# Kernel optimization log

Measured on AMD Instinct MI355X. Metric: run time of the kernel, lower is better.

The kernel has to match this reference:

```python
import jax, jax.numpy as jnp
import numpy as np

B, S, H = 2, 2048, 768
NH, HD = 12, 64
I = 1152
EPS = 1e-5
ROPE_BASE = 10000.0
MAX_POS = 8192


def _layernorm(x, w, b):
    mu = jnp.mean(x, axis=-1, keepdims=True)
    var = jnp.mean(jnp.square(x - mu), axis=-1, keepdims=True)
    return (x - mu) / jnp.sqrt(var + EPS) * w + b


def _rope_tables():
    pos = jnp.arange(MAX_POS, dtype=jnp.float32)
    theta = 1.0 / (ROPE_BASE ** (jnp.arange(0, HD, 2, dtype=jnp.float32) / HD))
    ang = pos[:, None] * theta  # [MAX_POS, HD//2]
    return jnp.cos(ang), jnp.sin(ang)


def _apply_rope(x, cos, sin):
    # x: [B, NH, S, HD]; cos/sin: [B, 1, S, HD//2]; interleaved pair rotation
    x2 = x.reshape(*x.shape[:-1], HD // 2, 2)
    x0, x1 = x2[..., 0], x2[..., 1]
    rot = jnp.stack([x0 * cos - x1 * sin, x1 * cos + x0 * sin], axis=-1)
    return rot.reshape(x.shape)


def setup_inputs() -> dict:
    key = jax.random.key(0)
    ks = jax.random.split(key, 8)
    std = 0.02
    return {
        "hidden_states": jax.random.normal(ks[0], (B, S, H), dtype=jnp.float32),
        "attention_mask": jnp.zeros((B, 1, S, S), dtype=jnp.float32),
        "sliding_window_mask": jnp.zeros((B, 1, S, S), dtype=jnp.float32),
        "position_ids": jnp.tile(jnp.arange(S, dtype=jnp.int32)[None, :], (B, 1)),
        "qkv_w": jax.random.normal(ks[1], (3 * H, H), dtype=jnp.float32) * std,
        "o_w": jax.random.normal(ks[2], (H, H), dtype=jnp.float32) * std,
        "attn_norm_w": jnp.ones((H,), dtype=jnp.float32),
        "attn_norm_b": jnp.zeros((H,), dtype=jnp.float32),
        "mlp_norm_w": jnp.ones((H,), dtype=jnp.float32),
        "mlp_norm_b": jnp.zeros((H,), dtype=jnp.float32),
        "wi_w": jax.random.normal(ks[3], (2 * I, H), dtype=jnp.float32) * std,
        "wi_b": jnp.zeros((2 * I,), dtype=jnp.float32),
        "wo_w": jax.random.normal(ks[4], (H, I), dtype=jnp.float32) * std,
        "wo_b": jnp.zeros((H,), dtype=jnp.float32),
    }


def reference(hidden_states, attention_mask, sliding_window_mask, position_ids,
              qkv_w, o_w, attn_norm_w, attn_norm_b, mlp_norm_w, mlp_norm_b,
              wi_w, wi_b, wo_w, wo_b):
    # --- attention block (layer_id != 0 -> pre-LN) ---
    x = _layernorm(hidden_states, attn_norm_w, attn_norm_b)
    qkv = jnp.einsum('bsh,oh->bso', x, qkv_w)          # [B,S,3H] (no bias)
    qkv = qkv.reshape(B, S, 3, NH, HD)
    qkv = jnp.transpose(qkv, (0, 3, 2, 1, 4))          # [B,NH,3,S,HD]
    q, k, v = qkv[:, :, 0], qkv[:, :, 1], qkv[:, :, 2]

    cos_t, sin_t = _rope_tables()
    cos = cos_t[position_ids][:, None]                 # [B,1,S,HD//2]
    sin = sin_t[position_ids][:, None]
    q = _apply_rope(q, cos, sin)
    k = _apply_rope(k, cos, sin)

    scale = HD ** -0.5
    scores = jnp.einsum('bhqd,bhkd->bhqk', q, k) * scale
    scores = scores + attention_mask + sliding_window_mask
    probs = jax.nn.softmax(scores, axis=-1)
    ctx = jnp.einsum('bhqk,bhkd->bhqd', probs, v)      # [B,NH,S,HD]
    ctx = jnp.transpose(ctx, (0, 2, 1, 3)).reshape(B, S, H)
    attn_out = jnp.einsum('bsh,oh->bso', ctx, o_w)
    hidden = hidden_states + attn_out

    # --- GeGLU MLP block ---
    y = _layernorm(hidden, mlp_norm_w, mlp_norm_b)
    h = jax.nn.gelu(jnp.einsum('bsh,oh->bso', y, wi_w) + wi_b, approximate=False)
    gated = h[..., 0::2] * h[..., 1::2]                # strided gelu-gate split
    mlp_out = jnp.einsum('bsi,oi->bso', gated, wo_w) + wo_b
    return hidden + mlp_out
```

## Files before the change

kernel.cpp:

```cpp
#include <hip/hip_runtime.h>
#include <hip/hip_bf16.h>
#include <math.h>

#define B_  2
#define S_  2048
#define H_  768
#define NH_ 12
#define HD_ 64
#define I_  1152
#define LOG2E 1.4426950408889634f
#define SCALE_L2E 0.18033688011112042f

typedef __bf16 bf16;
typedef __bf16 bf16x8 __attribute__((ext_vector_type(8)));
typedef float  f32x4  __attribute__((ext_vector_type(4)));
typedef float  f32x16 __attribute__((ext_vector_type(16)));
typedef float  f32x2  __attribute__((ext_vector_type(2)));
typedef unsigned u32x2 __attribute__((ext_vector_type(2)));
typedef unsigned u32x4 __attribute__((ext_vector_type(4)));

__device__ __forceinline__ void gll16(const void* g, void* l) {
  __builtin_amdgcn_global_load_lds((const __attribute__((address_space(1))) void*)g,
                                   (__attribute__((address_space(3))) void*)l, 16, 0, 0);
}

__device__ __forceinline__ unsigned pack_bf16(float a, float b) {
  union { bf16 e[2]; unsigned u; } r;
  r.e[0] = (bf16)a; r.e[1] = (bf16)b;
  return r.u;
}

__device__ __forceinline__ void plswap(unsigned &a, unsigned &b) {
  asm volatile("v_permlane32_swap_b32 %0, %1" : "+v"(a), "+v"(b));
}
__device__ __forceinline__ float halfmax(float x) {
  unsigned a = __builtin_bit_cast(unsigned, x), b = a;
  plswap(a, b);
  return fmaxf(__builtin_bit_cast(float, a), __builtin_bit_cast(float, b));
}
__device__ __forceinline__ float halfsum(float x) {
  unsigned a = __builtin_bit_cast(unsigned, x), b = a;
  plswap(a, b);
  return __builtin_bit_cast(float, a) + __builtin_bit_cast(float, b);
}

__global__ void cvt_f32_bf16(const float* __restrict__ in, bf16* __restrict__ out, int n4) {
  int i = blockIdx.x * 256 + threadIdx.x;
  if (i >= n4) return;
  float4 v = ((const float4*)in)[i];
  union { bf16 e[4]; uint2 u; } r;
  r.e[0] = (bf16)v.x; r.e[1] = (bf16)v.y; r.e[2] = (bf16)v.z; r.e[3] = (bf16)v.w;
  ((uint2*)out)[i] = r.u;
}

__global__ __launch_bounds__(256) void combine_mask2(const float* __restrict__ a,
                                                     const float* __restrict__ b,
                                                     bf16* __restrict__ E,
                                                     unsigned* __restrict__ flags) {
  const int kt = blockIdx.x, qi = blockIdx.y, bb = blockIdx.z, tid = threadIdx.x;
  float sm[8][4];
  bool ok = true;
#pragma unroll
  for (int c = 0; c < 8; ++c) {
    int idx4 = c * 256 + tid;
    int r = idx4 >> 4, col = (idx4 & 15) * 4;
    size_t g = ((size_t)(bb * S_) + qi * 128 + r) * S_ + kt * 64 + col;
    float4 x = *(const float4*)(a + g);
    float4 y = *(const float4*)(b + g);
    sm[c][0] = x.x + y.x; sm[c][1] = x.y + y.y;
    sm[c][2] = x.z + y.z; sm[c][3] = x.w + y.w;
    ok = ok && (sm[c][0] == 0.f) && (sm[c][1] == 0.f) && (sm[c][2] == 0.f) && (sm[c][3] == 0.f);
  }
  __shared__ unsigned sh[4];
  unsigned long long bal = __ballot(ok);
  if ((tid & 63) == 0) sh[tid >> 6] = (bal == ~0ull) ? 1u : 0u;
  __syncthreads();
  unsigned flag = sh[0] & sh[1] & sh[2] & sh[3];
  if (tid == 0) flags[(bb * 16 + qi) * 32 + kt] = flag;
  if (!flag) {
#pragma unroll
    for (int c = 0; c < 8; ++c) {
      int idx4 = c * 256 + tid;
      int r = idx4 >> 4, col = (idx4 & 15) * 4;
      size_t g = ((size_t)(bb * S_) + qi * 128 + r) * S_ + kt * 64 + col;
      union { bf16 e[4]; uint2 u; } w;
      w.e[0] = (bf16)__expf(sm[c][0]); w.e[1] = (bf16)__expf(sm[c][1]);
      w.e[2] = (bf16)__expf(sm[c][2]); w.e[3] = (bf16)__expf(sm[c][3]);
      *(uint2*)(E + g) = w.u;
    }
  }
}

__global__ __launch_bounds__(256) void ln_bf16(const float* __restrict__ in,
                                               const float* __restrict__ w,
                                               const float* __restrict__ bia,
                                               bf16* __restrict__ out) {
  int row = blockIdx.x, tid = threadIdx.x;
  const float* x = in + (size_t)row * H_;
  float v0 = x[tid], v1 = x[tid + 256], v2 = x[tid + 512];
  float s = v0 + v1 + v2;
  float q = v0 * v0 + v1 * v1 + v2 * v2;
  for (int o = 1; o < 64; o <<= 1) { s += __shfl_xor(s, o); q += __shfl_xor(q, o); }
  __shared__ float rs[4], rq[4];
  if ((tid & 63) == 0) { rs[tid >> 6] = s; rq[tid >> 6] = q; }
  __syncthreads();
  s = rs[0] + rs[1] + rs[2] + rs[3];
  q = rq[0] + rq[1] + rq[2] + rq[3];
  float mu = s * (1.f / H_);
  float var = q * (1.f / H_) - mu * mu;
  float rstd = rsqrtf(var + 1e-5f);
  bf16* orow = out + (size_t)row * H_;
  orow[tid]       = (bf16)((v0 - mu) * rstd * w[tid]       + bia[tid]);
  orow[tid + 256] = (bf16)((v1 - mu) * rstd * w[tid + 256] + bia[tid + 256]);
  orow[tid + 512] = (bf16)((v2 - mu) * rstd * w[tid + 512] + bia[tid + 512]);
}

template<bool BIAS, bool RES>
__global__ __launch_bounds__(256) void gemm128(const bf16* __restrict__ A,
                                               const bf16* __restrict__ W,
                                               float* __restrict__ C,
                                               const float* __restrict__ bias,
                                               const float* __restrict__ res,
                                               int M, int N, int K) {
  __shared__ bf16 As[128 * 32];
  __shared__ bf16 Bs[128 * 32];
  const int tid = threadIdx.x, lane = tid & 63, wv = tid >> 6;
  const int bm = blockIdx.y * 128, bn = blockIdx.x * 128;
  const int wr = (wv >> 1) * 64, wc = (wv & 1) * 64;
  const int l15 = lane & 15, lg = lane >> 4;

  f32x4 acc[4][4] = {};

  const int srow = tid >> 2, scc = (tid & 3) * 8;
  const bf16* aSrc0 = A + (size_t)(bm + srow) * K + scc;
  const bf16* aSrc1 = A + (size_t)(bm + 64 + srow) * K + scc;
  const bf16* bSrc0 = W + (size_t)(bn + srow) * K + scc;
  const bf16* bSrc1 = W + (size_t)(bn + 64 + srow) * K + scc;
  bf16* aDst0 = As + (size_t)tid * 8;
  bf16* aDst1 = As + (size_t)(256 + tid) * 8;
  bf16* bDst0 = Bs + (size_t)tid * 8;
  bf16* bDst1 = Bs + (size_t)(256 + tid) * 8;

  for (int k0 = 0; k0 < K; k0 += 32) {
    __syncthreads();
    gll16(aSrc0 + k0, aDst0);
    gll16(aSrc1 + k0, aDst1);
    gll16(bSrc0 + k0, bDst0);
    gll16(bSrc1 + k0, bDst1);
    __syncthreads();
    bf16x8 af[4], bfr[4];
#pragma unroll
    for (int i = 0; i < 4; ++i)
      af[i] = *(const bf16x8*)&As[(wr + i * 16 + l15) * 32 + lg * 8];
#pragma unroll
    for (int j = 0; j < 4; ++j)
      bfr[j] = *(const bf16x8*)&Bs[(wc + j * 16 + l15) * 32 + lg * 8];
#pragma unroll
    for (int i = 0; i < 4; ++i)
#pragma unroll
      for (int j = 0; j < 4; ++j)
        acc[i][j] = __builtin_amdgcn_mfma_f32_16x16x32_bf16(af[i], bfr[j], acc[i][j], 0, 0, 0);
  }

  const int r0 = lg * 4;
#pragma unroll
  for (int i = 0; i < 4; ++i) {
#pragma unroll
    for (int j = 0; j < 4; ++j) {
      int col = bn + wc + j * 16 + l15;
      float bv = BIAS ? bias[col] : 0.f;
#pragma unroll
      for (int r = 0; r < 4; ++r) {
        int row = bm + wr + i * 16 + r0 + r;
        float v = acc[i][j][r] + bv;
        if (RES) v += res[(size_t)row * N + col];
        C[(size_t)row * N + col] = v;
      }
    }
  }
}

__global__ void rope_split(const float* __restrict__ qkv, const int* __restrict__ pid,
                           bf16* __restrict__ Q, bf16* __restrict__ Kk, bf16* __restrict__ V) {
  int idx = blockIdx.x * 256 + threadIdx.x;
  int j = idx & 31;
  int row = idx >> 5;
  int s = row & (S_ - 1);
  int bh = row >> 11;
  int h = bh % NH_, b = bh / NH_;
  size_t src = (size_t)(b * S_ + s) * (3 * H_) + h * HD_ + 2 * j;
  f32x2 qv = *(const f32x2*)&qkv[src];
  f32x2 kv = *(const f32x2*)&qkv[src + H_];
  f32x2 vv = *(const f32x2*)&qkv[src + 2 * H_];
  int pos = pid[b * S_ + s];
  float th = exp2f((float)j * (-13.287712379549449f / 32.f));
  float ang = (float)pos * th;
  float sn, cs;
  sincosf(ang, &sn, &cs);
  size_t dst = ((size_t)(b * NH_ + h) * S_ + s) * HD_ + 2 * j;
  *(unsigned*)(Q + dst)  = pack_bf16(qv.x * cs - qv.y * sn, qv.y * cs + qv.x * sn);
  *(unsigned*)(Kk + dst) = pack_bf16(kv.x * cs - kv.y * sn, kv.y * cs + kv.x * sn);
  *(unsigned*)(V + dst)  = pack_bf16(vv.x, vv.y);
}

__global__ __launch_bounds__(512, 4) void attn8(
    const bf16* __restrict__ Q, const bf16* __restrict__ Kg, const bf16* __restrict__ Vg,
    const bf16* __restrict__ Eg, const unsigned* __restrict__ flags, bf16* __restrict__ ctx) {
  __shared__ bf16 Kt[2][2][64 * 64];
  __shared__ bf16 Vt[2][2][64 * 64];
  const int tid = threadIdx.x, lane = tid & 63, wv = tid >> 6;
  const int wq = wv & 3, ks = wv >> 2;
  const int qi = blockIdx.x, h = blockIdx.y, b = blockIdx.z;
  const int l31 = lane & 31, hi = lane >> 5, b4 = (lane >> 4) & 1;
  const size_t headbase = (size_t)(b * NH_ + h) * S_ * HD_;
  const bf16* kbase = Kg + headbase;
  const bf16* vbase = Vg + headbase;
  const unsigned* fptr = flags + (b * 16 + qi) * 32;
  const int kswz = (l31 & 7) << 4;
  const int qrow = qi * 128 + wq * 32 + l31;
  const bf16* Erow = Eg + (size_t)b * S_ * S_ + (size_t)qrow * S_;

  bf16x8 qf[4];
  {
    const bf16* qp = Q + headbase + (size_t)qrow * HD_;
#pragma unroll
    for (int kc = 0; kc < 4; ++kc)
      qf[kc] = *(const bf16x8*)(qp + kc * 16 + hi * 8);
  }

  auto stageK = [&](int t, int bs, int par) {
    int kr = tid >> 3, sl = tid & 7;
    gll16(kbase + (size_t)t * 64 * HD_ + kr * HD_ + (sl ^ (kr & 7)) * 8, &Kt[bs][par][tid * 8]);
  };
  auto stageV = [&](int t, int bs, int par) {
    int p = tid >> 7, kr = (tid & 127) >> 1, hf = tid & 1;
    gll16(vbase + (size_t)t * 64 * HD_ + kr * HD_ + (p >> 1) * 32 + (p & 1) * 16 + hf * 8,
          &Vt[bs][par][tid * 8]);
  };

  float m = -1e30f, l = 0.f;
  f32x16 oa[2] = {};

  stageK(0, 0, 0); stageV(0, 0, 0);
  stageK(1, 0, 1); stageV(1, 0, 1);
  unsigned fl = fptr[ks];
  __syncthreads();

  for (int r = 0; r < 16; ++r) {
    const int cur = r & 1;
    const int kt = 2 * r + ks;
    unsigned flN = 1;
    if (r < 15) {
      flN = fptr[kt + 2];
      stageK(2 * r + 2, cur ^ 1, 0); stageV(2 * r + 2, cur ^ 1, 0);
      stageK(2 * r + 3, cur ^ 1, 1); stageV(2 * r + 3, cur ^ 1, 1);
    }

    f32x16 sv[2];
    __builtin_amdgcn_s_setprio(1);
#pragma unroll
    for (int kb = 0; kb < 2; ++kb) {
      f32x16 s = {};
#pragma unroll
      for (int kc = 0; kc < 4; ++kc) {
        const bf16x8 kf = *(const bf16x8*)((const char*)&Kt[cur][ks][0] +
            ((kb * 32 + l31) * 128 + ((kc * 32 + hi * 16) ^ kswz)));
        s = __builtin_amdgcn_mfma_f32_32x32x16_bf16(kf, qf[kc], s, 0, 0, 0);
      }
      sv[kb] = s;
    }
    __builtin_amdgcn_s_setprio(0);

    float p0 = fmaxf(sv[0][0], sv[1][0]), p1 = fmaxf(sv[0][1], sv[1][1]);
    float p2 = fmaxf(sv[0][2], sv[1][2]), p3 = fmaxf(sv[0][3], sv[1][3]);
#pragma unroll
    for (int r2 = 4; r2 < 16; r2 += 4) {
      p0 = fmaxf(p0, fmaxf(sv[0][r2],     sv[1][r2]));
      p1 = fmaxf(p1, fmaxf(sv[0][r2 + 1], sv[1][r2 + 1]));
      p2 = fmaxf(p2, fmaxf(sv[0][r2 + 2], sv[1][r2 + 2]));
      p3 = fmaxf(p3, fmaxf(sv[0][r2 + 3], sv[1][r2 + 3]));
    }
    float pmS = halfmax(fmaxf(fmaxf(p0, p1), fmaxf(p2, p3))) * SCALE_L2E;
    if (__any(pmS - m > 8.f)) {
      float mn = fmaxf(m, pmS);
      float alpha = exp2f(m - mn);
      m = mn;
      l *= alpha;
#pragma unroll
      for (int db = 0; db < 2; ++db)
#pragma unroll
        for (int r2 = 0; r2 < 16; ++r2) oa[db][r2] *= alpha;
    }
#pragma unroll
    for (int kb = 0; kb < 2; ++kb)
#pragma unroll
      for (int r2 = 0; r2 < 16; ++r2)
        sv[kb][r2] = exp2f(fmaf(sv[kb][r2], SCALE_L2E, -m));
    if (!fl) {
#pragma unroll
      for (int kb = 0; kb < 2; ++kb)
#pragma unroll
        for (int rq = 0; rq < 4; ++rq) {
          union { bf16 e[4]; u32x2 u; } eu;
          eu.u = *(const u32x2*)(Erow + (size_t)kt * 64 + kb * 32 + rq * 8 + hi * 4);
#pragma unroll
          for (int j = 0; j < 4; ++j)
            sv[kb][rq * 4 + j] *= (float)eu.e[j];
        }
    }
    float s0 = sv[0][0] + sv[1][0], s1 = sv[0][1] + sv[1][1];
    float s2 = sv[0][2] + sv[1][2], s3 = sv[0][3] + sv[1][3];
#pragma unroll
    for (int r2 = 4; r2 < 16; r2 += 4) {
      s0 += sv[0][r2]     + sv[1][r2];
      s1 += sv[0][r2 + 1] + sv[1][r2 + 1];
      s2 += sv[0][r2 + 2] + sv[1][r2 + 2];
      s3 += sv[0][r2 + 3] + sv[1][r2 + 3];
    }
    l += halfsum((s0 + s1) + (s2 + s3));

    unsigned pk[2][4][2];
#pragma unroll
    for (int kb = 0; kb < 2; ++kb)
#pragma unroll
      for (int rq = 0; rq < 4; ++rq)
#pragma unroll
        for (int dd = 0; dd < 2; ++dd)
          pk[kb][rq][dd] = pack_bf16(sv[kb][rq * 4 + dd * 2], sv[kb][rq * 4 + dd * 2 + 1]);
    unsigned pa[4][4];
#pragma unroll
    for (int kc = 0; kc < 4; ++kc) {
      const int kb = kc >> 1, rb = (kc & 1) * 2;
#pragma unroll
      for (int dd = 0; dd < 2; ++dd) {
        unsigned A = pk[kb][rb][dd], Bv = pk[kb][rb + 1][dd];
        plswap(A, Bv);
        pa[kc][dd] = A; pa[kc][2 + dd] = Bv;
      }
    }

    const unsigned vlds = (unsigned)(size_t)&Vt[cur][ks][0] + b4 * 1920;
#pragma unroll
    for (int db = 0; db < 2; ++db) {
      u32x2 tr[4][2];
#pragma unroll
      for (int kc = 0; kc < 4; ++kc)
#pragma unroll
        for (int rd = 0; rd < 2; ++rd) {
          unsigned ad = vlds + (db * 4096 + kc * 512 + rd * 128);
          asm volatile("ds_read_b64_tr_b16 %0, %1 offset:0" : "=v"(tr[kc][rd]) : "v"(ad));
        }
      asm volatile("s_waitcnt lgkmcnt(0)" ::: "memory");
      __builtin_amdgcn_sched_barrier(0);
      __builtin_amdgcn_s_setprio(1);
#pragma unroll
      for (int kc = 0; kc < 4; ++kc) {
        union { u32x4 u; bf16x8 v; } vfu, pau;
        vfu.u = (u32x4){tr[kc][0][0], tr[kc][0][1], tr[kc][1][0], tr[kc][1][1]};
        pau.u = (u32x4){pa[kc][0], pa[kc][1], pa[kc][2], pa[kc][3]};
        oa[db] = __builtin_amdgcn_mfma_f32_32x32x16_bf16(vfu.v, pau.v, oa[db], 0, 0, 0);
      }
      __builtin_amdgcn_s_setprio(0);
    }
    __syncthreads();
    fl = flN;
  }

  float* KO = (float*)&Kt[0][0][0];
  float* ML = (float*)&Vt[1][0][0];
  if (ks == 1) {
#pragma unroll
    for (int db = 0; db < 2; ++db)
#pragma unroll
      for (int rq = 0; rq < 4; ++rq) {
        int q4 = (db * 4 + rq) ^ (l31 & 7);
        *(f32x4*)&KO[wq * 2048 + l31 * 64 + hi * 32 + q4 * 4] =
            (f32x4){oa[db][rq * 4], oa[db][rq * 4 + 1], oa[db][rq * 4 + 2], oa[db][rq * 4 + 3]};
      }
    if (hi == 0) { ML[wq * 64 + l31 * 2] = m; ML[wq * 64 + l31 * 2 + 1] = l; }
  }
  __syncthreads();
  if (ks == 0) {
    float m1 = ML[wq * 64 + l31 * 2], l1 = ML[wq * 64 + l31 * 2 + 1];
    float ms = fmaxf(m, m1);
    float a0 = exp2f(m - ms), a1 = exp2f(m1 - ms);
    float inv = 1.f / (l * a0 + l1 * a1);
    a0 *= inv; a1 *= inv;
    char* TR = (char*)&Vt[0][0][0];
#pragma unroll
    for (int db = 0; db < 2; ++db)
#pragma unroll
      for (int rq = 0; rq < 4; ++rq) {
        int q4 = (db * 4 + rq) ^ (l31 & 7);
        f32x4 o1 = *(const f32x4*)&KO[wq * 2048 + l31 * 64 + hi * 32 + q4 * 4];
        float f0 = oa[db][rq * 4 + 0] * a0 + o1[0] * a1;
        float f1 = oa[db][rq * 4 + 1] * a0 + o1[1] * a1;
        float f2 = oa[db][rq * 4 + 2] * a0 + o1[2] * a1;
        float f3 = oa[db][rq * 4 + 3] * a0 + o1[3] * a1;
        u32x2 w = (u32x2){pack_bf16(f0, f1), pack_bf16(f2, f3)};
        *(u32x2*)(TR + wq * 4096 + l31 * 128 + ((db * 64 + rq * 16 + hi * 8) ^ kswz)) = w;
      }
  }
  __syncthreads();
#pragma unroll
  for (int c = 0; c < 2; ++c) {
    int ch = c * 512 + tid, q = ch >> 3, sl = ch & 7;
    u32x4 vv = *(const u32x4*)((const char*)&Vt[0][0][0] +
        ((q >> 5) * 4096 + (q & 31) * 128 + ((sl ^ (q & 7)) * 16)));
    *(u32x4*)(ctx + ((size_t)(b * S_) + qi * 128 + q) * H_ + h * HD_ + sl * 8) = vv;
  }
}

__global__ void gelu_gate(const float* __restrict__ h, bf16* __restrict__ g, int n) {
  int i = blockIdx.x * 256 + threadIdx.x;
  if (i >= n) return;
  int row = i / I_, col = i % I_;
  f32x2 hv = *(const f32x2*)&h[(size_t)row * (2 * I_) + 2 * col];
  float g0 = 0.5f * hv.x * (1.f + erff(hv.x * 0.70710678118654752f));
  float g1 = 0.5f * hv.y * (1.f + erff(hv.y * 0.70710678118654752f));
  g[i] = (bf16)(g0 * g1);
}

extern "C" void kernel_launch(void* const* d_in, const int* in_sizes, int n_in,
                              void* d_out, int out_size, void* d_ws, size_t ws_size,
                              hipStream_t stream) {
  const float* hs   = (const float*)d_in[0];
  const float* am   = (const float*)d_in[1];
  const float* swm  = (const float*)d_in[2];
  const int*   pid  = (const int*)d_in[3];
  const float* qkvw = (const float*)d_in[4];
  const float* ow   = (const float*)d_in[5];
  const float* anw  = (const float*)d_in[6];
  const float* anb  = (const float*)d_in[7];
  const float* mnw  = (const float*)d_in[8];
  const float* mnb  = (const float*)d_in[9];
  const float* wiw  = (const float*)d_in[10];
  const float* wib  = (const float*)d_in[11];
  const float* wow  = (const float*)d_in[12];
  const float* wob  = (const float*)d_in[13];
  float* out = (float*)d_out;

  char* ws = (char*)d_ws;
  size_t off = 0;
  auto alloc = [&](size_t bytes) { void* p = ws + off; off += (bytes + 255) & ~255ull; return p; };

  bf16* wqkv_b = (bf16*)alloc((size_t)3 * H_ * H_ * 2);
  bf16* wo_b   = (bf16*)alloc((size_t)H_ * H_ * 2);
  bf16* wwi_b  = (bf16*)alloc((size_t)2 * I_ * H_ * 2);
  bf16* wwo_b  = (bf16*)alloc((size_t)H_ * I_ * 2);
  bf16* xln    = (bf16*)alloc((size_t)B_ * S_ * H_ * 2);
  float* qkvf  = (float*)alloc((size_t)B_ * S_ * 3 * H_ * 4);
  bf16* qb     = (bf16*)alloc((size_t)B_ * NH_ * S_ * HD_ * 2);
  bf16* kb     = (bf16*)alloc((size_t)B_ * NH_ * S_ * HD_ * 2);
  bf16* vb     = (bf16*)alloc((size_t)B_ * NH_ * S_ * HD_ * 2);
  bf16* Eg     = (bf16*)alloc((size_t)B_ * S_ * S_ * 2);
  unsigned* flg= (unsigned*)alloc((size_t)B_ * 16 * 32 * 4);
  bf16* ctx    = (bf16*)alloc((size_t)B_ * S_ * H_ * 2);
  float* hid2  = (float*)alloc((size_t)B_ * S_ * H_ * 4);
  bf16* gated  = (bf16*)alloc((size_t)B_ * S_ * I_ * 2);
  (void)ws_size; (void)n_in; (void)in_sizes; (void)out_size;

  const int rows = B_ * S_;

  cvt_f32_bf16<<<(3 * H_ * H_ / 4 + 255) / 256, 256, 0, stream>>>(qkvw, wqkv_b, 3 * H_ * H_ / 4);
  cvt_f32_bf16<<<(H_ * H_ / 4 + 255) / 256, 256, 0, stream>>>(ow, wo_b, H_ * H_ / 4);
  cvt_f32_bf16<<<(2 * I_ * H_ / 4 + 255) / 256, 256, 0, stream>>>(wiw, wwi_b, 2 * I_ * H_ / 4);
  cvt_f32_bf16<<<(H_ * I_ / 4 + 255) / 256, 256, 0, stream>>>(wow, wwo_b, H_ * I_ / 4);
  combine_mask2<<<dim3(32, 16, B_), 256, 0, stream>>>(am, swm, Eg, flg);

  ln_bf16<<<rows, 256, 0, stream>>>(hs, anw, anb, xln);
  gemm128<false, false><<<dim3(3 * H_ / 128, rows / 128), 256, 0, stream>>>(
      xln, wqkv_b, qkvf, nullptr, nullptr, rows, 3 * H_, H_);
  rope_split<<<B_ * NH_ * S_ * 32 / 256, 256, 0, stream>>>(qkvf, pid, qb, kb, vb);
  attn8<<<dim3(S_ / 128, NH_, B_), 512, 0, stream>>>(qb, kb, vb, Eg, flg, ctx);
  gemm128<false, true><<<dim3(H_ / 128, rows / 128), 256, 0, stream>>>(
      ctx, wo_b, hid2, nullptr, hs, rows, H_, H_);
  ln_bf16<<<rows, 256, 0, stream>>>(hid2, mnw, mnb, xln);
  gemm128<true, false><<<dim3(2 * I_ / 128, rows / 128), 256, 0, stream>>>(
      xln, wwi_b, qkvf, wib, nullptr, rows, 2 * I_, H_);
  gelu_gate<<<(rows * I_ + 255) / 256, 256, 0, stream>>>(qkvf, gated, rows * I_);
  gemm128<true, true><<<dim3(H_ / 128, rows / 128), 256, 0, stream>>>(
      gated, wwo_b, out, wob, hid2, rows, H_, I_);
}
```

Before: 241.0 us.

## Fuse RoPE and GeGLU into GEMM epilogues and double-buffer GEMM main loop

The QKV GEMM epilogue now applies RoPE, using a precomputed cos/sin table and a lane shuffle for the pair partner, and writes bf16 Q/K/V directly in head-major layout. The Wi GEMM epilogue now applies GELU and the gate product, writing the gated bf16 output. Both changes remove the fp32 intermediate round-trips and two elementwise kernels. The shared GEMM loop is also double-buffered with async global-to-LDS loads and MFMA priority hints, which doubles LDS use and adds a small table-build kernel.

```diff
diff --git a/kernel.cpp b/kernel.cpp
--- a/kernel.cpp
+++ b/kernel.cpp
@@ -51,6 +51,15 @@
   union { bf16 e[4]; uint2 u; } r;
   r.e[0] = (bf16)v.x; r.e[1] = (bf16)v.y; r.e[2] = (bf16)v.z; r.e[3] = (bf16)v.w;
   ((uint2*)out)[i] = r.u;
+}
+
+__global__ void build_rope_tbl(f32x2* __restrict__ tbl) {
+  int i = blockIdx.x * 256 + threadIdx.x;
+  int jp = i & 31, pos = i >> 5;
+  float th = exp2f((float)jp * (-13.287712379549449f / 32.f));
+  float sn, cs;
+  sincosf((float)pos * th, &sn, &cs);
+  tbl[i] = (f32x2){cs, sn};
 }
 
 __global__ __launch_bounds__(256) void combine_mask2(const float* __restrict__ a,
@@ -115,6 +124,46 @@
   orow[tid + 512] = (bf16)((v2 - mu) * rstd * w[tid + 512] + bia[tid + 512]);
 }
 
+__device__ __forceinline__ void gemm_main_loop(
+    int K, const bf16* __restrict__ aSrc0, const bf16* __restrict__ aSrc1,
+    const bf16* __restrict__ bSrc0, const bf16* __restrict__ bSrc1,
+    bf16* As, bf16* Bs, int tid, int wr, int wc, int l15, int lg,
+    f32x4 (&acc)[4][4]) {
+  const int NT = K >> 5;
+  auto stage = [&](int t, int buf) {
+    const int ko = t * 32;
+    bf16* ad = As + buf * 4096 + tid * 8;
+    bf16* bd = Bs + buf * 4096 + tid * 8;
+    gll16(aSrc0 + ko, ad);
+    gll16(aSrc1 + ko, ad + 2048);
+    gll16(bSrc0 + ko, bd);
+    gll16(bSrc1 + ko, bd + 2048);
+  };
+  stage(0, 0);
+  __syncthreads();
+  for (int t = 0; t < NT; ++t) {
+    const int cur = t & 1;
+    if (t + 1 < NT) stage(t + 1, cur ^ 1);
+    const bf16* Ab = As + cur * 4096;
+    const bf16* Bb = Bs + cur * 4096;
+    bf16x8 af[4], bfr[4];
+#pragma unroll
+    for (int i = 0; i < 4; ++i)
+      af[i] = *(const bf16x8*)&Ab[(wr + i * 16 + l15) * 32 + lg * 8];
+#pragma unroll
+    for (int j = 0; j < 4; ++j)
+      bfr[j] = *(const bf16x8*)&Bb[(wc + j * 16 + l15) * 32 + lg * 8];
+    __builtin_amdgcn_s_setprio(1);
+#pragma unroll
+    for (int i = 0; i < 4; ++i)
+#pragma unroll
+      for (int j = 0; j < 4; ++j)
+        acc[i][j] = __builtin_amdgcn_mfma_f32_16x16x32_bf16(af[i], bfr[j], acc[i][j], 0, 0, 0);
+    __builtin_amdgcn_s_setprio(0);
+    __syncthreads();
+  }
+}
+
 template<bool BIAS, bool RES>
 __global__ __launch_bounds__(256) void gemm128(const bf16* __restrict__ A,
                                                const bf16* __restrict__ W,
@@ -122,45 +171,19 @@
                                                const float* __restrict__ bias,
                                                const float* __restrict__ res,
                                                int M, int N, int K) {
-  __shared__ bf16 As[128 * 32];
-  __shared__ bf16 Bs[128 * 32];
+  __shared__ bf16 As[2 * 128 * 32];
+  __shared__ bf16 Bs[2 * 128 * 32];
   const int tid = threadIdx.x, lane = tid & 63, wv = tid >> 6;
   const int bm = blockIdx.y * 128, bn = blockIdx.x * 128;
   const int wr = (wv >> 1) * 64, wc = (wv & 1) * 64;
   const int l15 = lane & 15, lg = lane >> 4;
 
   f32x4 acc[4][4] = {};
-
   const int srow = tid >> 2, scc = (tid & 3) * 8;
-  const bf16* aSrc0 = A + (size_t)(bm + srow) * K + scc;
-  const bf16* aSrc1 = A + (size_t)(bm + 64 + srow) * K + scc;
-  const bf16* bSrc0 = W + (size_t)(bn + srow) * K + scc;
-  const bf16* bSrc1 = W + (size_t)(bn + 64 + srow) * K + scc;
-  bf16* aDst0 = As + (size_t)tid * 8;
-  bf16* aDst1 = As + (size_t)(256 + tid) * 8;
-  bf16* bDst0 = Bs + (size_t)tid * 8;
-  bf16* bDst1 = Bs + (size_t)(256 + tid) * 8;
-
-  for (int k0 = 0; k0 < K; k0 += 32) {
-    __syncthreads();
-    gll16(aSrc0 + k0, aDst0);
-    gll16(aSrc1 + k0, aDst1);
-    gll16(bSrc0 + k0, bDst0);
-    gll16(bSrc1 + k0, bDst1);
-    __syncthreads();
-    bf16x8 af[4], bfr[4];
-#pragma unroll
-    for (int i = 0; i < 4; ++i)
-      af[i] = *(const bf16x8*)&As[(wr + i * 16 + l15) * 32 + lg * 8];
-#pragma unroll
-    for (int j = 0; j < 4; ++j)
-      bfr[j] = *(const bf16x8*)&Bs[(wc + j * 16 + l15) * 32 + lg * 8];
-#pragma unroll
-    for (int i = 0; i < 4; ++i)
-#pragma unroll
-      for (int j = 0; j < 4; ++j)
-        acc[i][j] = __builtin_amdgcn_mfma_f32_16x16x32_bf16(af[i], bfr[j], acc[i][j], 0, 0, 0);
-  }
+  gemm_main_loop(K,
+      A + (size_t)(bm + srow) * K + scc, A + (size_t)(bm + 64 + srow) * K + scc,
+      W + (size_t)(bn + srow) * K + scc, W + (size_t)(bn + 64 + srow) * K + scc,
+      As, Bs, tid, wr, wc, l15, lg, acc);
 
   const int r0 = lg * 4;
 #pragma unroll
@@ -180,27 +203,95 @@
   }
 }
 
-__global__ void rope_split(const float* __restrict__ qkv, const int* __restrict__ pid,
-                           bf16* __restrict__ Q, bf16* __restrict__ Kk, bf16* __restrict__ V) {
-  int idx = blockIdx.x * 256 + threadIdx.x;
-  int j = idx & 31;
-  int row = idx >> 5;
-  int s = row & (S_ - 1);
-  int bh = row >> 11;
-  int h = bh % NH_, b = bh / NH_;
-  size_t src = (size_t)(b * S_ + s) * (3 * H_) + h * HD_ + 2 * j;
-  f32x2 qv = *(const f32x2*)&qkv[src];
-  f32x2 kv = *(const f32x2*)&qkv[src + H_];
-  f32x2 vv = *(const f32x2*)&qkv[src + 2 * H_];
-  int pos = pid[b * S_ + s];
-  float th = exp2f((float)j * (-13.287712379549449f / 32.f));
-  float ang = (float)pos * th;
-  float sn, cs;
-  sincosf(ang, &sn, &cs);
-  size_t dst = ((size_t)(b * NH_ + h) * S_ + s) * HD_ + 2 * j;
-  *(unsigned*)(Q + dst)  = pack_bf16(qv.x * cs - qv.y * sn, qv.y * cs + qv.x * sn);
-  *(unsigned*)(Kk + dst) = pack_bf16(kv.x * cs - kv.y * sn, kv.y * cs + kv.x * sn);
-  *(unsigned*)(V + dst)  = pack_bf16(vv.x, vv.y);
+__global__ __launch_bounds__(256) void gemm_qkv(const bf16* __restrict__ A,
+                                                const bf16* __restrict__ W,
+                                                const int* __restrict__ pid,
+                                                const f32x2* __restrict__ tbl,
+                                                bf16* __restrict__ qb,
+                                                bf16* __restrict__ kb,
+                                                bf16* __restrict__ vb) {
+  __shared__ bf16 As[2 * 128 * 32];
+  __shared__ bf16 Bs[2 * 128 * 32];
+  const int tid = threadIdx.x, lane = tid & 63, wv = tid >> 6;
+  const int bm = blockIdx.y * 128, bn = blockIdx.x * 128;
+  const int wr = (wv >> 1) * 64, wc = (wv & 1) * 64;
+  const int l15 = lane & 15, lg = lane >> 4;
+  const int K = H_;
+
+  f32x4 acc[4][4] = {};
+  const int srow = tid >> 2, scc = (tid & 3) * 8;
+  gemm_main_loop(K,
+      A + (size_t)(bm + srow) * K + scc, A + (size_t)(bm + 64 + srow) * K + scc,
+      W + (size_t)(bn + srow) * K + scc, W + (size_t)(bn + 64 + srow) * K + scc,
+      As, Bs, tid, wr, wc, l15, lg, acc);
+
+  const int r0 = lg * 4;
+  const int sect = bn / H_;
+  const int hcb = (bn % H_) + wc;
+  bf16* dst0 = sect == 0 ? qb : (sect == 1 ? kb : vb);
+#pragma unroll
+  for (int i = 0; i < 4; ++i) {
+#pragma unroll
+    for (int r = 0; r < 4; ++r) {
+      const int row = bm + wr + i * 16 + r0 + r;
+      const int b = row >> 11, s = row & 2047;
+      const int pos = (sect < 2) ? pid[row] : 0;
+#pragma unroll
+      for (int j = 0; j < 4; ++j) {
+        const int hc = hcb + j * 16 + l15;
+        const int h = hc >> 6, d = hc & 63;
+        float x = acc[i][j][r];
+        float v;
+        if (sect < 2) {
+          f32x2 cs = tbl[pos * 32 + (d >> 1)];
+          float xp = __shfl_xor(x, 1);
+          v = (d & 1) ? fmaf(x, cs.x, xp * cs.y) : fmaf(x, cs.x, -xp * cs.y);
+        } else {
+          v = x;
+        }
+        dst0[((size_t)(b * NH_ + h) * S_ + s) * HD_ + d] = (bf16)v;
+      }
+    }
+  }
+}
+
+__global__ __launch_bounds__(256) void gemm_wi(const bf16* __restrict__ A,
+                                               const bf16* __restrict__ W,
+                                               const float* __restrict__ bias,
+                                               bf16* __restrict__ g) {
+  __shared__ bf16 As[2 * 128 * 32];
+  __shared__ bf16 Bs[2 * 128 * 32];
+  const int tid = threadIdx.x, lane = tid & 63, wv = tid >> 6;
+  const int bm = blockIdx.y * 128, bn = blockIdx.x * 128;
+  const int wr = (wv >> 1) * 64, wc = (wv & 1) * 64;
+  const int l15 = lane & 15, lg = lane >> 4;
+  const int K = H_;
+
+  f32x4 acc[4][4] = {};
+  const int srow = tid >> 2, scc = (tid & 3) * 8;
+  gemm_main_loop(K,
+      A + (size_t)(bm + srow) * K + scc, A + (size_t)(bm + 64 + srow) * K + scc,
+      W + (size_t)(bn + srow) * K + scc, W + (size_t)(bn + 64 + srow) * K + scc,
+      As, Bs, tid, wr, wc, l15, lg, acc);
+
+  const int r0 = lg * 4;
+#pragma unroll
+  for (int j = 0; j < 4; ++j) {
+    const int col = bn + wc + j * 16 + l15;
+    const float bv = bias[col];
+#pragma unroll
+    for (int i = 0; i < 4; ++i) {
+#pragma unroll
+      for (int r = 0; r < 4; ++r) {
+        const int row = bm + wr + i * 16 + r0 + r;
+        float x = acc[i][j][r] + bv;
+        float gx = 0.5f * x * (1.f + erff(x * 0.70710678118654752f));
+        float gp = __shfl_xor(gx, 1);
+        if (!(l15 & 1))
+          g[(size_t)row * I_ + (col >> 1)] = (bf16)(gx * gp);
+      }
+    }
+  }
 }
 
 __global__ __launch_bounds__(512, 4) void attn8(
@@ -409,16 +500,6 @@
         ((q >> 5) * 4096 + (q & 31) * 128 + ((sl ^ (q & 7)) * 16)));
     *(u32x4*)(ctx + ((size_t)(b * S_) + qi * 128 + q) * H_ + h * HD_ + sl * 8) = vv;
   }
-}
-
-__global__ void gelu_gate(const float* __restrict__ h, bf16* __restrict__ g, int n) {
-  int i = blockIdx.x * 256 + threadIdx.x;
-  if (i >= n) return;
-  int row = i / I_, col = i % I_;
-  f32x2 hv = *(const f32x2*)&h[(size_t)row * (2 * I_) + 2 * col];
-  float g0 = 0.5f * hv.x * (1.f + erff(hv.x * 0.70710678118654752f));
-  float g1 = 0.5f * hv.y * (1.f + erff(hv.y * 0.70710678118654752f));
-  g[i] = (bf16)(g0 * g1);
 }
 
 extern "C" void kernel_launch(void* const* d_in, const int* in_sizes, int n_in,
@@ -449,7 +530,6 @@
   bf16* wwi_b  = (bf16*)alloc((size_t)2 * I_ * H_ * 2);
   bf16* wwo_b  = (bf16*)alloc((size_t)H_ * I_ * 2);
   bf16* xln    = (bf16*)alloc((size_t)B_ * S_ * H_ * 2);
-  float* qkvf  = (float*)alloc((size_t)B_ * S_ * 3 * H_ * 4);
   bf16* qb     = (bf16*)alloc((size_t)B_ * NH_ * S_ * HD_ * 2);
   bf16* kb     = (bf16*)alloc((size_t)B_ * NH_ * S_ * HD_ * 2);
   bf16* vb     = (bf16*)alloc((size_t)B_ * NH_ * S_ * HD_ * 2);
@@ -458,6 +538,7 @@
   bf16* ctx    = (bf16*)alloc((size_t)B_ * S_ * H_ * 2);
   float* hid2  = (float*)alloc((size_t)B_ * S_ * H_ * 4);
   bf16* gated  = (bf16*)alloc((size_t)B_ * S_ * I_ * 2);
+  f32x2* tbl   = (f32x2*)alloc((size_t)8192 * 32 * 8);
   (void)ws_size; (void)n_in; (void)in_sizes; (void)out_size;
 
   const int rows = B_ * S_;
@@ -466,19 +547,17 @@
   cvt_f32_bf16<<<(H_ * H_ / 4 + 255) / 256, 256, 0, stream>>>(ow, wo_b, H_ * H_ / 4);
   cvt_f32_bf16<<<(2 * I_ * H_ / 4 + 255) / 256, 256, 0, stream>>>(wiw, wwi_b, 2 * I_ * H_ / 4);
   cvt_f32_bf16<<<(H_ * I_ / 4 + 255) / 256, 256, 0, stream>>>(wow, wwo_b, H_ * I_ / 4);
+  build_rope_tbl<<<8192 * 32 / 256, 256, 0, stream>>>(tbl);
   combine_mask2<<<dim3(32, 16, B_), 256, 0, stream>>>(am, swm, Eg, flg);
 
   ln_bf16<<<rows, 256, 0, stream>>>(hs, anw, anb, xln);
-  gemm128<false, false><<<dim3(3 * H_ / 128, rows / 128), 256, 0, stream>>>(
-      xln, wqkv_b, qkvf, nullptr, nullptr, rows, 3 * H_, H_);
-  rope_split<<<B_ * NH_ * S_ * 32 / 256, 256, 0, stream>>>(qkvf, pid, qb, kb, vb);
+  gemm_qkv<<<dim3(3 * H_ / 128, rows / 128), 256, 0, stream>>>(
+      xln, wqkv_b, pid, tbl, qb, kb, vb);
   attn8<<<dim3(S_ / 128, NH_, B_), 512, 0, stream>>>(qb, kb, vb, Eg, flg, ctx);
   gemm128<false, true><<<dim3(H_ / 128, rows / 128), 256, 0, stream>>>(
       ctx, wo_b, hid2, nullptr, hs, rows, H_, H_);
   ln_bf16<<<rows, 256, 0, stream>>>(hid2, mnw, mnb, xln);
-  gemm128<true, false><<<dim3(2 * I_ / 128, rows / 128), 256, 0, stream>>>(
-      xln, wwi_b, qkvf, wib, nullptr, rows, 2 * I_, H_);
-  gelu_gate<<<(rows * I_ + 255) / 256, 256, 0, stream>>>(qkvf, gated, rows * I_);
+  gemm_wi<<<dim3(2 * I_ / 128, rows / 128), 256, 0, stream>>>(xln, wwi_b, wib, gated);
   gemm128<true, true><<<dim3(H_ / 128, rows / 128), 256, 0, stream>>>(
       gated, wwo_b, out, wob, hid2, rows, H_, I_);
 }
```

New measurement: 233.1 us. 3.3% less time.
